# Optimization experiments

Measured on AMD Instinct MI355X. Metric: run time of the kernel, lower is better.

The kernel has to match this reference:

```python
import jax, jax.numpy as jnp
from jax import lax
import numpy as np

T, B, D, N = 1024, 32, 1024, 64
INIT_D_ALPHA, INIT_ALPHA_BIAS = 0.1, 2.0

def _xavier(key, n_out, n_in):
    lim = float(np.sqrt(6.0 / (n_in + n_out)))
    return jax.random.uniform(key, (n_out, n_in), jnp.float32, -lim, lim)

def setup_inputs() -> dict:
    key = jax.random.key(0)
    k = jax.random.split(key, 5)
    return {
        "x": jax.random.normal(k[0], (T, B, D), jnp.float32),
        "S0": jnp.zeros((B, N, N), jnp.float32),
        "W_k": _xavier(k[1], N, D),
        "W_v": _xavier(k[2], N, D),
        "W_q": _xavier(k[3], N, D),
        "W_alpha": _xavier(k[4], N, D),
        "d_alpha": jnp.full((N,), INIT_D_ALPHA, jnp.float32),
        "b_alpha": jnp.full((N,), INIT_ALPHA_BIAS, jnp.float32),
    }

def reference(x, S0, W_k, W_v, W_q, W_alpha, d_alpha, b_alpha):
    # Precompute all per-step projections as batched GEMMs: [T,B,N]
    k = jnp.einsum('tbd,nd->tbn', x, W_k)
    v = jnp.einsum('tbd,nd->tbn', x, W_v)
    q = jnp.einsum('tbd,nd->tbn', x, W_q)
    ax = jnp.einsum('tbd,nd->tbn', x, W_alpha)

    def step(S, inp):
        k_t, v_t, q_t, ax_t = inp  # each [B,N]
        retrieved = jnp.einsum('bij,bj->bi', S, k_t)            # S @ k
        alpha = jax.nn.sigmoid(ax_t + d_alpha * retrieved + b_alpha)  # [B,N]
        outer = v_t[:, :, None] * k_t[:, None, :]               # outer(v,k) [B,N,N]
        S = alpha[:, :, None] * S + (1.0 - alpha)[:, :, None] * outer
        h = jnp.einsum('bij,bj->bi', S, q_t)                    # S @ q
        out = h * jax.nn.silu(h)                                # self-gated
        return S, out

    S_final, output = lax.scan(step, S0, (k, v, q, ax))
    return output, S_final
```

## Files before the change

### kernel.cpp

```cpp
#include <hip/hip_runtime.h>
#include <math.h>

#define T_STEPS 1024
#define BATCH   32
#define DIM     1024
#define NST     64
#define TBN     ((size_t)T_STEPS * BATCH * NST)

typedef __attribute__((ext_vector_type(8))) short bf16x8;
typedef __attribute__((ext_vector_type(4))) float f32x4;


__device__ __forceinline__ void gload16(const float* g, float* l)
{
    __builtin_amdgcn_global_load_lds(
        (const __attribute__((address_space(1))) unsigned int*)g,
        (__attribute__((address_space(3))) unsigned int*)l, 16, 0, 0);
}

__device__ __forceinline__ void cvt8(float4 v0, float4 v1, bf16x8& hi, bf16x8& lo)
{
    float f[8] = {v0.x, v0.y, v0.z, v0.w, v1.x, v1.y, v1.z, v1.w};
    bf16x8 h, l;
    #pragma unroll
    for (int i = 0; i < 8; i++) {
        unsigned b = __float_as_uint(f[i]);
        h[i] = (short)(b >> 16);
        l[i] = (short)(__float_as_uint(f[i] - __uint_as_float(b & 0xffff0000u)) >> 16);
    }
    hi = h; lo = l;
}

__global__ __launch_bounds__(512, 1)
void proj_gemm_v2(const float* __restrict__ x,
                  const float* __restrict__ Wk,
                  const float* __restrict__ Wv,
                  const float* __restrict__ Wq,
                  const float* __restrict__ Wa,
                  const float* __restrict__ b_alpha,
                  float* __restrict__ ws)
{
    __shared__ float As[2][128][32];
    __shared__ float Bs[2][256][32];

    const int tid  = threadIdx.x;
    const int lane = tid & 63;
    const int w    = tid >> 6;
    const int m0   = blockIdx.x * 128;

    const int lrow  = lane >> 3;
    const int lgran = (lane & 7) ^ lrow;
    const float* ap0 = x + (size_t)(m0 + 16*w +     lrow) * DIM + lgran * 4;
    const float* ap1 = x + (size_t)(m0 + 16*w + 8 + lrow) * DIM + lgran * 4;
    const float* Wsrc = (w < 2) ? Wk : (w < 4) ? Wv : (w < 6) ? Wq : Wa;
    const float* bp0 = Wsrc + (size_t)((w & 1)*32 +  0 + lrow) * DIM + lgran * 4;
    const float* bp1 = Wsrc + (size_t)((w & 1)*32 +  8 + lrow) * DIM + lgran * 4;
    const float* bp2 = Wsrc + (size_t)((w & 1)*32 + 16 + lrow) * DIM + lgran * 4;
    const float* bp3 = Wsrc + (size_t)((w & 1)*32 + 24 + lrow) * DIM + lgran * 4;

    auto stage = [&](int kb, int buf) {
        const int ko = kb * 32;
        gload16(ap0 + ko, &As[buf][16*w     ][0]);
        gload16(ap1 + ko, &As[buf][16*w +  8][0]);
        gload16(bp0 + ko, &Bs[buf][32*w     ][0]);
        gload16(bp1 + ko, &Bs[buf][32*w +  8][0]);
        gload16(bp2 + ko, &Bs[buf][32*w + 16][0]);
        gload16(bp3 + ko, &Bs[buf][32*w + 24][0]);
    };

    const int fr = lane & 15;
    const int qi = lane >> 4;
    const int sx = fr & 7;
    const int mh = w >> 2;
    const int nq = w & 3;

    f32x4 acc[4][4];
    #pragma unroll
    for (int i = 0; i < 4; i++)
        #pragma unroll
        for (int j = 0; j < 4; j++)
            acc[i][j] = (f32x4)0.0f;

    stage(0, 0);
    __syncthreads();

    #pragma unroll 1
    for (int kb = 0; kb < 32; kb++) {
        const int buf = kb & 1;
        if (kb + 1 < 32) stage(kb + 1, buf ^ 1);

        bf16x8 ah[4], al[4], bh[4], bl[4];
        #pragma unroll
        for (int mt = 0; mt < 4; mt++) {
            const float* rp = &As[buf][mh*64 + mt*16 + fr][0];
            float4 v0 = *(const float4*)(rp + (((2*qi    ) ^ sx) * 4));
            float4 v1 = *(const float4*)(rp + (((2*qi + 1) ^ sx) * 4));
            cvt8(v0, v1, ah[mt], al[mt]);
        }
        #pragma unroll
        for (int nt = 0; nt < 4; nt++) {
            const float* rp = &Bs[buf][nq*64 + nt*16 + fr][0];
            float4 v0 = *(const float4*)(rp + (((2*qi    ) ^ sx) * 4));
            float4 v1 = *(const float4*)(rp + (((2*qi + 1) ^ sx) * 4));
            cvt8(v0, v1, bh[nt], bl[nt]);
        }
        #pragma unroll
        for (int mt = 0; mt < 4; mt++)
            #pragma unroll
            for (int nt = 0; nt < 4; nt++) {
                acc[mt][nt] = __builtin_amdgcn_mfma_f32_16x16x32_bf16(ah[mt], bh[nt], acc[mt][nt], 0, 0, 0);
                acc[mt][nt] = __builtin_amdgcn_mfma_f32_16x16x32_bf16(al[mt], bh[nt], acc[mt][nt], 0, 0, 0);
                acc[mt][nt] = __builtin_amdgcn_mfma_f32_16x16x32_bf16(ah[mt], bl[nt], acc[mt][nt], 0, 0, 0);
            }

        __syncthreads();
    }

    float* outb = ws + (size_t)nq * TBN;
    const int r0 = qi * 4;
    float bav[4];
    #pragma unroll
    for (int nt = 0; nt < 4; nt++)
        bav[nt] = (nq == 3) ? b_alpha[nt*16 + fr] : 0.0f;
    #pragma unroll
    for (int mt = 0; mt < 4; mt++)
        #pragma unroll
        for (int nt = 0; nt < 4; nt++)
            #pragma unroll
            for (int r = 0; r < 4; r++)
                outb[(size_t)(m0 + mh*64 + mt*16 + r0 + r) * NST + nt*16 + fr]
                    = acc[mt][nt][r] + bav[nt];
}


template <int CTRL>
__device__ __forceinline__ float dpp_add(float v) {
    int o = __builtin_amdgcn_mov_dpp(__float_as_int(v), CTRL, 0xF, 0xF, true);
    return v + __int_as_float(o);
}
__device__ __forceinline__ float reduce16(float v) {
    v = dpp_add<0xB1>(v);
    v = dpp_add<0x4E>(v);
    v = dpp_add<0x141>(v);
    v = dpp_add<0x140>(v);
    return v;
}
__device__ __forceinline__ float fast_sigmoid(float z) {
    float e = __builtin_amdgcn_exp2f(z * -1.44269504088896340736f);
    return __builtin_amdgcn_rcpf(1.0f + e);
}

#define SCH 16
#define NCH (T_STEPS / SCH)

__global__ __launch_bounds__(64, 1)
void scan16_kernel(const float* __restrict__ ws,
                   const float* __restrict__ S0,
                   const float* __restrict__ d_alpha,
                   float* __restrict__ out)
{
    const float* kb_ = ws;
    const float* vb_ = ws + TBN;
    const float* qb_ = ws + 2 * TBN;
    const float* ab_ = ws + 3 * TBN;

    __shared__ float kq[2][SCH][128];
    __shared__ float va[2][SCH][8];
    __shared__ float dd[SCH];

    const int lane = threadIdx.x;
    const int bid = blockIdx.x;
    const int b   = (bid & 7) * 4 + ((bid >> 3) & 3);
    const int rg  = bid >> 5;
    const int rl  = lane >> 4;
    const int cl  = lane & 15;
    const int row = rg * 4 + rl;
    const int c0  = cl * 4;

    float S[4];
    {
        float4 sv = *(const float4*)(S0 + ((size_t)b * NST + row) * NST + c0);
        S[0] = sv.x; S[1] = sv.y; S[2] = sv.z; S[3] = sv.w;
    }
    const float da = d_alpha[row];

    const size_t stp = (size_t)BATCH * NST;

    int kqs[8], kqf[8];
    const float* kqg[8];
    #pragma unroll
    for (int p = 0; p < 8; p++) {
        const int idx = p * 64 + lane;
        const int s   = idx >> 5;
        const int f   = idx & 31;
        kqs[p] = s; kqf[p] = f;
        kqg[p] = ((f < 16) ? kb_ : qb_) + (size_t)s * stp + (size_t)b * NST + (f & 15) * 4;
    }
    const int vas = (lane & 31) >> 1;
    const int vaw = lane & 1;
    const float* vag = (vaw ? ab_ : vb_) + (size_t)vas * stp + (size_t)b * NST + rg * 4;

    auto issue = [&](int ch, float4 (&rk)[8], float4& rv) {
        const size_t off = (size_t)ch * SCH * stp;
        #pragma unroll
        for (int p = 0; p < 8; p++)
            rk[p] = *(const float4*)(kqg[p] + off);
        rv = *(const float4*)(vag + off);
    };
    auto commit = [&](int bi, const float4 (&rk)[8], const float4& rv) {
        #pragma unroll
        for (int p = 0; p < 8; p++)
            *(float4*)&kq[bi][kqs[p]][kqf[p] * 4] = rk[p];
        if (lane < 32)
            *(float4*)&va[bi][vas][vaw * 4] = rv;
    };

    {
        float4 rk[8]; float4 rv;
        issue(0, rk, rv); commit(0, rk, rv);
        issue(1, rk, rv); commit(1, rk, rv);
    }

    float kc[4], kn[4];
    *(float4*)kc = *(const float4*)&kq[0][0][c0];
    *(float4*)kn = *(const float4*)&kq[0][1][c0];
    float qf_c[4];
    *(float4*)qf_c = *(const float4*)&kq[0][0][64 + c0];
    float vv_c = va[0][0][rl];
    float aa_c = va[0][0][4 + rl];

    float ret;
    {
        float p0 = fmaf(S[1], kc[1], S[0] * kc[0]) + fmaf(S[3], kc[3], S[2] * kc[2]);
        ret = reduce16(p0);
    }

    float* op = out + (size_t)b * NST + row;

    for (int ch = 0; ch < NCH; ch++) {
        const int cur = ch & 1, nxt = cur ^ 1;

        float4 rk[8]; float4 rv;
        const int cn = (ch + 2 < NCH) ? ch + 2 : NCH - 1;
        issue(cn, rk, rv);

        {
            const int tl = lane & 15;
            const int qg = lane >> 4;
            const float* kt = &kq[cur][tl][0];
            const float* knp = (tl < 15) ? &kq[cur][tl + 1][0] : &kq[nxt][0][0];
            float dsum = 0.0f;
            #pragma unroll
            for (int i = 0; i < 4; i++) {
                const int g = ((qg * 4 + i + tl) & 15) * 4;
                float4 a = *(const float4*)(kt + g);
                float4 c = *(const float4*)(knp + g);
                dsum = fmaf(a.x, c.x, dsum); dsum = fmaf(a.y, c.y, dsum);
                dsum = fmaf(a.z, c.z, dsum); dsum = fmaf(a.w, c.w, dsum);
            }
            dsum += __shfl_xor(dsum, 16);
            dsum += __shfl_xor(dsum, 32);
            if (lane < 16) dd[lane] = dsum;
        }

        #pragma unroll
        for (int s = 0; s < SCH; s++) {
            const int t = ch * SCH + s;

            float qf_n[4], kn2[4], vv_n, aa_n;
            if (s < SCH - 1) {
                *(float4*)qf_n = *(const float4*)&kq[cur][s + 1][64 + c0];
                vv_n = va[cur][s + 1][rl];
                aa_n = va[cur][s + 1][4 + rl];
            } else {
                *(float4*)qf_n = *(const float4*)&kq[nxt][0][64 + c0];
                vv_n = va[nxt][0][rl];
                aa_n = va[nxt][0][4 + rl];
            }
            if (s < SCH - 2)       *(float4*)kn2 = *(const float4*)&kq[cur][s + 2][c0];
            else if (s == SCH - 2) *(float4*)kn2 = *(const float4*)&kq[nxt][0][c0];
            else                   *(float4*)kn2 = *(const float4*)&kq[nxt][1][c0];

            const float d2v = dd[s];

            const float z     = fmaf(da, ret, aa_c);
            const float alpha = fast_sigmoid(z);

            float d1 = fmaf(S[1], kn[1], S[0] * kn[0]) + fmaf(S[3], kn[3], S[2] * kn[2]);
            d1 = reduce16(d1);

            const float w = (1.f - alpha) * vv_c;
            S[0] = fmaf(alpha, S[0], w * kc[0]);
            S[1] = fmaf(alpha, S[1], w * kc[1]);
            S[2] = fmaf(alpha, S[2], w * kc[2]);
            S[3] = fmaf(alpha, S[3], w * kc[3]);

            const float c2v = vv_c * d2v;
            ret = fmaf(alpha, d1 - c2v, c2v);

            float h = fmaf(S[1], qf_c[1], S[0] * qf_c[0]) + fmaf(S[3], qf_c[3], S[2] * qf_c[2]);
            h = reduce16(h);
            const float o = h * h * fast_sigmoid(h);
            if (cl == 0) op[(size_t)t * stp] = o;

            kc[0] = kn[0]; kc[1] = kn[1]; kc[2] = kn[2]; kc[3] = kn[3];
            kn[0] = kn2[0]; kn[1] = kn2[1]; kn[2] = kn2[2]; kn[3] = kn2[3];
            qf_c[0] = qf_n[0]; qf_c[1] = qf_n[1]; qf_c[2] = qf_n[2]; qf_c[3] = qf_n[3];
            vv_c = vv_n; aa_c = aa_n;
        }

        commit(cur, rk, rv);
    }

    float* sfp = out + TBN + ((size_t)b * NST + row) * NST + c0;
    *(float4*)sfp = make_float4(S[0], S[1], S[2], S[3]);
}


extern "C" void kernel_launch(void* const* d_in, const int* in_sizes, int n_in,
                              void* d_out, int out_size, void* d_ws, size_t ws_size,
                              hipStream_t stream)
{
    const float* x  = (const float*)d_in[0];
    const float* S0 = (const float*)d_in[1];
    const float* Wk = (const float*)d_in[2];
    const float* Wv = (const float*)d_in[3];
    const float* Wq = (const float*)d_in[4];
    const float* Wa = (const float*)d_in[5];
    const float* da = (const float*)d_in[6];
    const float* ba = (const float*)d_in[7];
    float* out = (float*)d_out;
    float* ws  = (float*)d_ws;

    proj_gemm_v2<<<dim3((T_STEPS * BATCH) / 128), 512, 0, stream>>>(x, Wk, Wv, Wq, Wa, ba, ws);

    scan16_kernel<<<dim3(BATCH * 16), 64, 0, stream>>>(ws, S0, da, out);
}
```

Baseline: 408.7 us.

## Deepen retrieval recurrence lookahead to two steps and batch output reductions

```diff
diff --git a/kernel.cpp b/kernel.cpp
--- a/kernel.cpp
+++ b/kernel.cpp
@@ -9,6 +9,8 @@
 
 typedef __attribute__((ext_vector_type(8))) short bf16x8;
 typedef __attribute__((ext_vector_type(4))) float f32x4;
+
+#define NLOG2E (-1.44269504088896340736f)
 
 
 __device__ __forceinline__ void gload16(const float* g, float* l)
@@ -122,6 +124,7 @@
     #pragma unroll
     for (int nt = 0; nt < 4; nt++)
         bav[nt] = (nq == 3) ? b_alpha[nt*16 + fr] : 0.0f;
+    const float scl = (nq == 3) ? NLOG2E : 1.0f;
     #pragma unroll
     for (int mt = 0; mt < 4; mt++)
         #pragma unroll
@@ -129,7 +132,7 @@
             #pragma unroll
             for (int r = 0; r < 4; r++)
                 outb[(size_t)(m0 + mh*64 + mt*16 + r0 + r) * NST + nt*16 + fr]
-                    = acc[mt][nt][r] + bav[nt];
+                    = (acc[mt][nt][r] + bav[nt]) * scl;
 }
 
 
@@ -145,9 +148,18 @@
     v = dpp_add<0x140>(v);
     return v;
 }
-__device__ __forceinline__ float fast_sigmoid(float z) {
-    float e = __builtin_amdgcn_exp2f(z * -1.44269504088896340736f);
+__device__ __forceinline__ void reduce16x4(float& a, float& b, float& c, float& d) {
+    a = dpp_add<0xB1>(a);  b = dpp_add<0xB1>(b);  c = dpp_add<0xB1>(c);  d = dpp_add<0xB1>(d);
+    a = dpp_add<0x4E>(a);  b = dpp_add<0x4E>(b);  c = dpp_add<0x4E>(c);  d = dpp_add<0x4E>(d);
+    a = dpp_add<0x141>(a); b = dpp_add<0x141>(b); c = dpp_add<0x141>(c); d = dpp_add<0x141>(d);
+    a = dpp_add<0x140>(a); b = dpp_add<0x140>(b); c = dpp_add<0x140>(c); d = dpp_add<0x140>(d);
+}
+__device__ __forceinline__ float fast_sigmoid(float h) {
+    float e = __builtin_amdgcn_exp2f(h * NLOG2E);
     return __builtin_amdgcn_rcpf(1.0f + e);
+}
+__device__ __forceinline__ float dot4(const float* a, const float* b) {
+    return fmaf(a[1], b[1], a[0] * b[0]) + fmaf(a[3], b[3], a[2] * b[2]);
 }
 
 #define SCH 16
@@ -166,7 +178,7 @@
 
     __shared__ float kq[2][SCH][128];
     __shared__ float va[2][SCH][8];
-    __shared__ float dd[SCH];
+    __shared__ float ddt[SCH], eet[SCH];
 
     const int lane = threadIdx.x;
     const int bid = blockIdx.x;
@@ -182,7 +194,7 @@
         float4 sv = *(const float4*)(S0 + ((size_t)b * NST + row) * NST + c0);
         S[0] = sv.x; S[1] = sv.y; S[2] = sv.z; S[3] = sv.w;
     }
-    const float da = d_alpha[row];
+    const float da_s = d_alpha[row] * NLOG2E;
 
     const size_t stp = (size_t)BATCH * NST;
 
@@ -221,22 +233,25 @@
         issue(1, rk, rv); commit(1, rk, rv);
     }
 
-    float kc[4], kn[4];
-    *(float4*)kc = *(const float4*)&kq[0][0][c0];
-    *(float4*)kn = *(const float4*)&kq[0][1][c0];
-    float qf_c[4];
+    float kc[4], kn[4], kn2[4];
+    *(float4*)kc  = *(const float4*)&kq[0][0][c0];
+    *(float4*)kn  = *(const float4*)&kq[0][1][c0];
+    *(float4*)kn2 = *(const float4*)&kq[0][2][c0];
+    float qf_c[4], qf_n[4];
     *(float4*)qf_c = *(const float4*)&kq[0][0][64 + c0];
-    float vv_c = va[0][0][rl];
-    float aa_c = va[0][0][4 + rl];
-
-    float ret;
-    {
-        float p0 = fmaf(S[1], kc[1], S[0] * kc[0]) + fmaf(S[3], kc[3], S[2] * kc[2]);
-        ret = reduce16(p0);
-    }
-
+    *(float4*)qf_n = *(const float4*)&kq[0][1][64 + c0];
+    float vv_c = va[0][0][rl], aa_c = va[0][0][4 + rl];
+    float vv_n = va[0][1][rl], aa_n = va[0][1][4 + rl];
+
+    float a1 = 1.0f, oma1 = 0.0f, vprev = 0.0f, eev_carry = 0.0f;
+    float gg = 0.0f;
+    float u  = reduce16(dot4(S, kc));
+    float RD = reduce16(dot4(S, kn));
+
+    float hp[4];
     float* op = out + (size_t)b * NST + row;
 
+    #pragma unroll 1
     for (int ch = 0; ch < NCH; ch++) {
         const int cur = ch & 1, nxt = cur ^ 1;
 
@@ -247,68 +262,99 @@
         {
             const int tl = lane & 15;
             const int qg = lane >> 4;
-            const float* kt = &kq[cur][tl][0];
-            const float* knp = (tl < 15) ? &kq[cur][tl + 1][0] : &kq[nxt][0][0];
-            float dsum = 0.0f;
+            const float* k0p = &kq[cur][tl][0];
+            const float* k1p = (tl < 15) ? &kq[cur][tl + 1][0] : &kq[nxt][0][0];
+            const float* k2p = (tl < 14) ? &kq[cur][tl + 2][0] : &kq[nxt][tl - 14][0];
+            float ds = 0.0f, es = 0.0f;
             #pragma unroll
             for (int i = 0; i < 4; i++) {
                 const int g = ((qg * 4 + i + tl) & 15) * 4;
-                float4 a = *(const float4*)(kt + g);
-                float4 c = *(const float4*)(knp + g);
-                dsum = fmaf(a.x, c.x, dsum); dsum = fmaf(a.y, c.y, dsum);
-                dsum = fmaf(a.z, c.z, dsum); dsum = fmaf(a.w, c.w, dsum);
+                float4 a  = *(const float4*)(k0p + g);
+                float4 b1 = *(const float4*)(k1p + g);
+                float4 c  = *(const float4*)(k2p + g);
+                ds = fmaf(a.x, b1.x, ds); ds = fmaf(a.y, b1.y, ds);
+                ds = fmaf(a.z, b1.z, ds); ds = fmaf(a.w, b1.w, ds);
+                es = fmaf(a.x, c.x, es);  es = fmaf(a.y, c.y, es);
+                es = fmaf(a.z, c.z, es);  es = fmaf(a.w, c.w, es);
             }
-            dsum += __shfl_xor(dsum, 16);
-            dsum += __shfl_xor(dsum, 32);
-            if (lane < 16) dd[lane] = dsum;
+            ds += __shfl_xor(ds, 16); ds += __shfl_xor(ds, 32);
+            es += __shfl_xor(es, 16); es += __shfl_xor(es, 32);
+            if (lane < 16) { ddt[lane] = ds; eet[lane] = es; }
+        }
+        float ddRa[16], eeRa[16];
+        #pragma unroll
+        for (int j = 0; j < 4; j++) {
+            *(float4*)&ddRa[4*j] = *(const float4*)&ddt[4*j];
+            *(float4*)&eeRa[4*j] = *(const float4*)&eet[4*j];
         }
 
         #pragma unroll
         for (int s = 0; s < SCH; s++) {
             const int t = ch * SCH + s;
 
-            float qf_n[4], kn2[4], vv_n, aa_n;
-            if (s < SCH - 1) {
-                *(float4*)qf_n = *(const float4*)&kq[cur][s + 1][64 + c0];
-                vv_n = va[cur][s + 1][rl];
-                aa_n = va[cur][s + 1][4 + rl];
+            const float ret = fmaf(a1, gg, u);
+            const float z   = fmaf(da_s, ret, aa_c);
+            const float e   = __builtin_amdgcn_exp2f(z);
+
+            float k3[4], qn2[4], vv2, aa2;
+            if (s + 3 < SCH) *(float4*)k3 = *(const float4*)&kq[cur][s + 3][c0];
+            else             *(float4*)k3 = *(const float4*)&kq[nxt][s + 3 - SCH][c0];
+            if (s + 2 < SCH) {
+                *(float4*)qn2 = *(const float4*)&kq[cur][s + 2][64 + c0];
+                vv2 = va[cur][s + 2][rl]; aa2 = va[cur][s + 2][4 + rl];
             } else {
-                *(float4*)qf_n = *(const float4*)&kq[nxt][0][64 + c0];
-                vv_n = va[nxt][0][rl];
-                aa_n = va[nxt][0][4 + rl];
+                *(float4*)qn2 = *(const float4*)&kq[nxt][s + 2 - SCH][64 + c0];
+                vv2 = va[nxt][s + 2 - SCH][rl]; aa2 = va[nxt][s + 2 - SCH][4 + rl];
             }
-            if (s < SCH - 2)       *(float4*)kn2 = *(const float4*)&kq[cur][s + 2][c0];
-            else if (s == SCH - 2) *(float4*)kn2 = *(const float4*)&kq[nxt][0][c0];
-            else                   *(float4*)kn2 = *(const float4*)&kq[nxt][1][c0];
-
-            const float d2v = dd[s];
-
-            const float z     = fmaf(da, ret, aa_c);
-            const float alpha = fast_sigmoid(z);
-
-            float d1 = fmaf(S[1], kn[1], S[0] * kn[0]) + fmaf(S[3], kn[3], S[2] * kn[2]);
-            d1 = reduce16(d1);
-
-            const float w = (1.f - alpha) * vv_c;
+
+            const float ddv = ddRa[s];
+            const float eev = (s == 0) ? eev_carry : eeRa[s - 1];
+            const float w1  = oma1 * vprev * eev;
+            const float P   = fmaf(a1, RD, w1);
+            const float u_n = vv_c * ddv;
+            const float gg_n = P - u_n;
+
+            float qp = dot4(S, kn2);
+            const float RD_n = reduce16(qp);
+
+            const float alpha = __builtin_amdgcn_rcpf(1.0f + e);
+
+            const float oma = 1.0f - alpha;
+            const float w   = oma * vv_c;
             S[0] = fmaf(alpha, S[0], w * kc[0]);
             S[1] = fmaf(alpha, S[1], w * kc[1]);
             S[2] = fmaf(alpha, S[2], w * kc[2]);
             S[3] = fmaf(alpha, S[3], w * kc[3]);
 
-            const float c2v = vv_c * d2v;
-            ret = fmaf(alpha, d1 - c2v, c2v);
-
-            float h = fmaf(S[1], qf_c[1], S[0] * qf_c[0]) + fmaf(S[3], qf_c[3], S[2] * qf_c[2]);
-            h = reduce16(h);
-            const float o = h * h * fast_sigmoid(h);
-            if (cl == 0) op[(size_t)t * stp] = o;
-
-            kc[0] = kn[0]; kc[1] = kn[1]; kc[2] = kn[2]; kc[3] = kn[3];
+            hp[s & 3] = dot4(S, qf_c);
+            if ((s & 3) == 3) {
+                float h0 = hp[0], h1 = hp[1], h2 = hp[2], h3 = hp[3];
+                reduce16x4(h0, h1, h2, h3);
+                const float o0 = h0 * h0 * fast_sigmoid(h0);
+                const float o1 = h1 * h1 * fast_sigmoid(h1);
+                const float o2 = h2 * h2 * fast_sigmoid(h2);
+                const float o3 = h3 * h3 * fast_sigmoid(h3);
+                if (cl == 0) {
+                    op[(size_t)(t - 3) * stp] = o0;
+                    op[(size_t)(t - 2) * stp] = o1;
+                    op[(size_t)(t - 1) * stp] = o2;
+                    op[(size_t)(t    ) * stp] = o3;
+                }
+            }
+
+            a1 = alpha; oma1 = oma; vprev = vv_c;
+            u = u_n; gg = gg_n;
+            float RDt = RD_n; (void)RDt;
+            kc[0] = kn[0];  kc[1] = kn[1];  kc[2] = kn[2];  kc[3] = kn[3];
             kn[0] = kn2[0]; kn[1] = kn2[1]; kn[2] = kn2[2]; kn[3] = kn2[3];
+            kn2[0] = k3[0]; kn2[1] = k3[1]; kn2[2] = k3[2]; kn2[3] = k3[3];
             qf_c[0] = qf_n[0]; qf_c[1] = qf_n[1]; qf_c[2] = qf_n[2]; qf_c[3] = qf_n[3];
-            vv_c = vv_n; aa_c = aa_n;
-        }
-
+            qf_n[0] = qn2[0];  qf_n[1] = qn2[1];  qf_n[2] = qn2[2];  qf_n[3] = qn2[3];
+            vv_c = vv_n; aa_c = aa_n; vv_n = vv2; aa_n = aa2;
+            RD = RD_n;
+        }
+
+        eev_carry = eeRa[15];
         commit(cur, rk, rv);
     }
 
```

Measured after the change: 416.6 us. No clear change (+1.9%).

## Chunked Gram-matrix scan with MFMA retrieval and output projections

Applied to the files above, without the earlier changes.

```diff
diff --git a/kernel.cpp b/kernel.cpp
--- a/kernel.cpp
+++ b/kernel.cpp
@@ -9,6 +9,13 @@
 
 typedef __attribute__((ext_vector_type(8))) short bf16x8;
 typedef __attribute__((ext_vector_type(4))) float f32x4;
+
+#define NLOG2E (-1.44269504088896340736f)
+
+__device__ unsigned short g_khi[TBN];
+__device__ unsigned short g_klo[TBN];
+__device__ unsigned short g_qhi[TBN];
+__device__ unsigned short g_qlo[TBN];
 
 
 __device__ __forceinline__ void gload16(const float* g, float* l)
@@ -122,198 +129,179 @@
     #pragma unroll
     for (int nt = 0; nt < 4; nt++)
         bav[nt] = (nq == 3) ? b_alpha[nt*16 + fr] : 0.0f;
+    const float scl = (nq == 3) ? NLOG2E : 1.0f;
     #pragma unroll
     for (int mt = 0; mt < 4; mt++)
         #pragma unroll
         for (int nt = 0; nt < 4; nt++)
             #pragma unroll
-            for (int r = 0; r < 4; r++)
-                outb[(size_t)(m0 + mh*64 + mt*16 + r0 + r) * NST + nt*16 + fr]
-                    = acc[mt][nt][r] + bav[nt];
-}
-
-
-template <int CTRL>
-__device__ __forceinline__ float dpp_add(float v) {
-    int o = __builtin_amdgcn_mov_dpp(__float_as_int(v), CTRL, 0xF, 0xF, true);
-    return v + __int_as_float(o);
-}
-__device__ __forceinline__ float reduce16(float v) {
-    v = dpp_add<0xB1>(v);
-    v = dpp_add<0x4E>(v);
-    v = dpp_add<0x141>(v);
-    v = dpp_add<0x140>(v);
-    return v;
-}
-__device__ __forceinline__ float fast_sigmoid(float z) {
-    float e = __builtin_amdgcn_exp2f(z * -1.44269504088896340736f);
-    return __builtin_amdgcn_rcpf(1.0f + e);
-}
+            for (int r = 0; r < 4; r++) {
+                const float val = (acc[mt][nt][r] + bav[nt]) * scl;
+                const size_t idx = (size_t)(m0 + mh*64 + mt*16 + r0 + r) * NST + nt*16 + fr;
+                if (nq != 2)
+                    outb[idx] = val;
+                if (nq == 0 || nq == 2) {
+                    const unsigned bits = __float_as_uint(val);
+                    const unsigned short hi = (unsigned short)(bits >> 16);
+                    const float lof = val - __uint_as_float(bits & 0xffff0000u);
+                    const unsigned short lo = (unsigned short)(__float_as_uint(lof) >> 16);
+                    if (nq == 0) { g_khi[idx] = hi; g_klo[idx] = lo; }
+                    else         { g_qhi[idx] = hi; g_qlo[idx] = lo; }
+                }
+            }
+}
+
 
 #define SCH 16
 #define NCH (T_STEPS / SCH)
 
-__global__ __launch_bounds__(64, 1)
-void scan16_kernel(const float* __restrict__ ws,
-                   const float* __restrict__ S0,
-                   const float* __restrict__ d_alpha,
-                   float* __restrict__ out)
+__global__ __launch_bounds__(256, 2)
+void scan_gram(const float* __restrict__ ws,
+               const float* __restrict__ S0,
+               const float* __restrict__ d_alpha,
+               float* __restrict__ out)
 {
     const float* kb_ = ws;
     const float* vb_ = ws + TBN;
-    const float* qb_ = ws + 2 * TBN;
     const float* ab_ = ws + 3 * TBN;
 
-    __shared__ float kq[2][SCH][128];
-    __shared__ float va[2][SCH][8];
-    __shared__ float dd[SCH];
-
-    const int lane = threadIdx.x;
-    const int bid = blockIdx.x;
-    const int b   = (bid & 7) * 4 + ((bid >> 3) & 3);
-    const int rg  = bid >> 5;
-    const int rl  = lane >> 4;
-    const int cl  = lane & 15;
-    const int row = rg * 4 + rl;
-    const int c0  = cl * 4;
-
-    float S[4];
-    {
-        float4 sv = *(const float4*)(S0 + ((size_t)b * NST + row) * NST + c0);
-        S[0] = sv.x; S[1] = sv.y; S[2] = sv.z; S[3] = sv.w;
+    __shared__ float k_st[2][SCH][64];
+    __shared__ float va  [2][SCH][16];
+    __shared__ float G_lds [SCH][16];
+    __shared__ float GQ_lds[SCH][16];
+    __shared__ float S_pvt[4][64];
+
+    const int tid  = threadIdx.x;
+    const int lane = tid & 63;
+    const int w    = tid >> 6;
+    const int bid  = blockIdx.x;
+    const int b    = (bid & 7) * 4 + ((bid >> 3) & 3);
+    const int rg   = bid >> 5;
+    const int row  = rg * 4 + w;
+    const int fr   = lane & 15;
+    const int qi   = lane >> 4;
+
+    const size_t stp = (size_t)BATCH * NST;
+
+    float S = S0[((size_t)b * NST + row) * NST + lane];
+    const float da_s = d_alpha[row] * NLOG2E;
+
+    const float* ksrc = kb_ + (size_t)(4*w + qi) * stp + (size_t)b * NST + fr * 4;
+    const float* vsrc = ((lane & 1) ? ab_ : vb_)
+                      + (size_t)(lane >> 2) * stp + (size_t)b * NST + rg * 4;
+
+    auto stage = [&](int ch, int buf) {
+        gload16(ksrc + (size_t)ch * SCH * stp, &k_st[buf][4*w][0]);
+        if (w == 0)
+            gload16(vsrc + (size_t)ch * SCH * stp, &va[buf][0][0]);
+    };
+
+    stage(0, 0);
+    __syncthreads();
+
+    float* op = out + (size_t)b * NST + row;
+    float R = 0.0f, H = 0.0f, hv = 0.0f;
+
+    #pragma unroll 1
+    for (int ch = 0; ch < NCH; ch++) {
+        const int buf = ch & 1;
+        if (ch + 1 < NCH) stage(ch + 1, buf ^ 1);
+
+        const size_t fb = (size_t)ch * SCH * stp + (size_t)fr * stp + (size_t)b * NST + qi * 8;
+        const bf16x8 Kh0 = *(const bf16x8*)(g_khi + fb);
+        const bf16x8 Kh1 = *(const bf16x8*)(g_khi + fb + 32);
+        const bf16x8 Kl0 = *(const bf16x8*)(g_klo + fb);
+        const bf16x8 Kl1 = *(const bf16x8*)(g_klo + fb + 32);
+        const bf16x8 Qh0 = *(const bf16x8*)(g_qhi + fb);
+        const bf16x8 Qh1 = *(const bf16x8*)(g_qhi + fb + 32);
+        const bf16x8 Ql0 = *(const bf16x8*)(g_qlo + fb);
+        const bf16x8 Ql1 = *(const bf16x8*)(g_qlo + fb + 32);
+
+        S_pvt[w][lane] = S;
+        bf16x8 Sh0, Sl0, Sh1, Sl1;
+        {
+            float4 s0 = *(const float4*)&S_pvt[w][qi * 8];
+            float4 s1 = *(const float4*)&S_pvt[w][qi * 8 + 4];
+            cvt8(s0, s1, Sh0, Sl0);
+            float4 s2 = *(const float4*)&S_pvt[w][32 + qi * 8];
+            float4 s3 = *(const float4*)&S_pvt[w][32 + qi * 8 + 4];
+            cvt8(s2, s3, Sh1, Sl1);
+        }
+
+        f32x4 aG = (f32x4)0.0f, aGQ = (f32x4)0.0f;
+        f32x4 aR0 = (f32x4)0.0f, aR1 = (f32x4)0.0f;
+        f32x4 aH0 = (f32x4)0.0f, aH1 = (f32x4)0.0f;
+
+        aG = __builtin_amdgcn_mfma_f32_16x16x32_bf16(Kh0, Kh0, aG, 0, 0, 0);
+        aG = __builtin_amdgcn_mfma_f32_16x16x32_bf16(Kh0, Kl0, aG, 0, 0, 0);
+        aG = __builtin_amdgcn_mfma_f32_16x16x32_bf16(Kl0, Kh0, aG, 0, 0, 0);
+        aG = __builtin_amdgcn_mfma_f32_16x16x32_bf16(Kh1, Kh1, aG, 0, 0, 0);
+        aG = __builtin_amdgcn_mfma_f32_16x16x32_bf16(Kh1, Kl1, aG, 0, 0, 0);
+        aG = __builtin_amdgcn_mfma_f32_16x16x32_bf16(Kl1, Kh1, aG, 0, 0, 0);
+
+        aGQ = __builtin_amdgcn_mfma_f32_16x16x32_bf16(Kh0, Qh0, aGQ, 0, 0, 0);
+        aGQ = __builtin_amdgcn_mfma_f32_16x16x32_bf16(Kh0, Ql0, aGQ, 0, 0, 0);
+        aGQ = __builtin_amdgcn_mfma_f32_16x16x32_bf16(Kl0, Qh0, aGQ, 0, 0, 0);
+        aGQ = __builtin_amdgcn_mfma_f32_16x16x32_bf16(Kh1, Qh1, aGQ, 0, 0, 0);
+        aGQ = __builtin_amdgcn_mfma_f32_16x16x32_bf16(Kh1, Ql1, aGQ, 0, 0, 0);
+        aGQ = __builtin_amdgcn_mfma_f32_16x16x32_bf16(Kl1, Qh1, aGQ, 0, 0, 0);
+
+        aR0 = __builtin_amdgcn_mfma_f32_16x16x32_bf16(Sh0, Kh0, aR0, 0, 0, 0);
+        aR0 = __builtin_amdgcn_mfma_f32_16x16x32_bf16(Sh0, Kl0, aR0, 0, 0, 0);
+        aR0 = __builtin_amdgcn_mfma_f32_16x16x32_bf16(Sl0, Kh0, aR0, 0, 0, 0);
+        aR1 = __builtin_amdgcn_mfma_f32_16x16x32_bf16(Sh1, Kh1, aR1, 0, 0, 0);
+        aR1 = __builtin_amdgcn_mfma_f32_16x16x32_bf16(Sh1, Kl1, aR1, 0, 0, 0);
+        aR1 = __builtin_amdgcn_mfma_f32_16x16x32_bf16(Sl1, Kh1, aR1, 0, 0, 0);
+
+        aH0 = __builtin_amdgcn_mfma_f32_16x16x32_bf16(Sh0, Qh0, aH0, 0, 0, 0);
+        aH0 = __builtin_amdgcn_mfma_f32_16x16x32_bf16(Sh0, Ql0, aH0, 0, 0, 0);
+        aH0 = __builtin_amdgcn_mfma_f32_16x16x32_bf16(Sl0, Qh0, aH0, 0, 0, 0);
+        aH1 = __builtin_amdgcn_mfma_f32_16x16x32_bf16(Sh1, Qh1, aH1, 0, 0, 0);
+        aH1 = __builtin_amdgcn_mfma_f32_16x16x32_bf16(Sh1, Ql1, aH1, 0, 0, 0);
+        aH1 = __builtin_amdgcn_mfma_f32_16x16x32_bf16(Sl1, Qh1, aH1, 0, 0, 0);
+
+        #pragma unroll
+        for (int r = 0; r < 4; r++) {
+            G_lds [qi*4 + r][fr] = aG[r];
+            GQ_lds[qi*4 + r][fr] = aGQ[r];
+        }
+        R = aR0[0] + aR1[0];
+        H = aH0[0] + aH1[0];
+
+        #pragma unroll
+        for (int s = 0; s < SCH; s++) {
+            const float kcv = k_st[buf][s][lane];
+            const float Gv  = G_lds [s][fr];
+            const float GQv = GQ_lds[s][fr];
+            const float vv  = va[buf][s][w];
+            const float aa  = va[buf][s][4 + w];
+
+            const float ret   = __int_as_float(
+                __builtin_amdgcn_readlane(__float_as_int(R), s));
+            const float z     = fmaf(da_s, ret, aa);
+            const float e     = __builtin_amdgcn_exp2f(z);
+            const float alpha = __builtin_amdgcn_rcpf(1.0f + e);
+            const float bt    = (1.0f - alpha) * vv;
+
+            R = fmaf(alpha, R, bt * Gv);
+            H = fmaf(alpha, H, bt * GQv);
+            S = fmaf(alpha, S, bt * kcv);
+
+            hv = (lane == s) ? H : hv;
+        }
+
+        {
+            const float zz = hv * NLOG2E;
+            const float sg = __builtin_amdgcn_rcpf(1.0f + __builtin_amdgcn_exp2f(zz));
+            const float o  = hv * hv * sg;
+            if (lane < SCH)
+                op[(size_t)(ch * SCH + lane) * stp] = o;
+        }
+
+        __syncthreads();
     }
-    const float da = d_alpha[row];
-
-    const size_t stp = (size_t)BATCH * NST;
-
-    int kqs[8], kqf[8];
-    const float* kqg[8];
-    #pragma unroll
-    for (int p = 0; p < 8; p++) {
-        const int idx = p * 64 + lane;
-        const int s   = idx >> 5;
-        const int f   = idx & 31;
-        kqs[p] = s; kqf[p] = f;
-        kqg[p] = ((f < 16) ? kb_ : qb_) + (size_t)s * stp + (size_t)b * NST + (f & 15) * 4;
-    }
-    const int vas = (lane & 31) >> 1;
-    const int vaw = lane & 1;
-    const float* vag = (vaw ? ab_ : vb_) + (size_t)vas * stp + (size_t)b * NST + rg * 4;
-
-    auto issue = [&](int ch, float4 (&rk)[8], float4& rv) {
-        const size_t off = (size_t)ch * SCH * stp;
-        #pragma unroll
-        for (int p = 0; p < 8; p++)
-            rk[p] = *(const float4*)(kqg[p] + off);
-        rv = *(const float4*)(vag + off);
-    };
-    auto commit = [&](int bi, const float4 (&rk)[8], const float4& rv) {
-        #pragma unroll
-        for (int p = 0; p < 8; p++)
-            *(float4*)&kq[bi][kqs[p]][kqf[p] * 4] = rk[p];
-        if (lane < 32)
-            *(float4*)&va[bi][vas][vaw * 4] = rv;
-    };
-
-    {
-        float4 rk[8]; float4 rv;
-        issue(0, rk, rv); commit(0, rk, rv);
-        issue(1, rk, rv); commit(1, rk, rv);
-    }
-
-    float kc[4], kn[4];
-    *(float4*)kc = *(const float4*)&kq[0][0][c0];
-    *(float4*)kn = *(const float4*)&kq[0][1][c0];
-    float qf_c[4];
-    *(float4*)qf_c = *(const float4*)&kq[0][0][64 + c0];
-    float vv_c = va[0][0][rl];
-    float aa_c = va[0][0][4 + rl];
-
-    float ret;
-    {
-        float p0 = fmaf(S[1], kc[1], S[0] * kc[0]) + fmaf(S[3], kc[3], S[2] * kc[2]);
-        ret = reduce16(p0);
-    }
-
-    float* op = out + (size_t)b * NST + row;
-
-    for (int ch = 0; ch < NCH; ch++) {
-        const int cur = ch & 1, nxt = cur ^ 1;
-
-        float4 rk[8]; float4 rv;
-        const int cn = (ch + 2 < NCH) ? ch + 2 : NCH - 1;
-        issue(cn, rk, rv);
-
-        {
-            const int tl = lane & 15;
-            const int qg = lane >> 4;
-            const float* kt = &kq[cur][tl][0];
-            const float* knp = (tl < 15) ? &kq[cur][tl + 1][0] : &kq[nxt][0][0];
-            float dsum = 0.0f;
-            #pragma unroll
-            for (int i = 0; i < 4; i++) {
-                const int g = ((qg * 4 + i + tl) & 15) * 4;
-                float4 a = *(const float4*)(kt + g);
-                float4 c = *(const float4*)(knp + g);
-                dsum = fmaf(a.x, c.x, dsum); dsum = fmaf(a.y, c.y, dsum);
-                dsum = fmaf(a.z, c.z, dsum); dsum = fmaf(a.w, c.w, dsum);
-            }
-            dsum += __shfl_xor(dsum, 16);
-            dsum += __shfl_xor(dsum, 32);
-            if (lane < 16) dd[lane] = dsum;
-        }
-
-        #pragma unroll
-        for (int s = 0; s < SCH; s++) {
-            const int t = ch * SCH + s;
-
-            float qf_n[4], kn2[4], vv_n, aa_n;
-            if (s < SCH - 1) {
-                *(float4*)qf_n = *(const float4*)&kq[cur][s + 1][64 + c0];
-                vv_n = va[cur][s + 1][rl];
-                aa_n = va[cur][s + 1][4 + rl];
-            } else {
-                *(float4*)qf_n = *(const float4*)&kq[nxt][0][64 + c0];
-                vv_n = va[nxt][0][rl];
-                aa_n = va[nxt][0][4 + rl];
-            }
-            if (s < SCH - 2)       *(float4*)kn2 = *(const float4*)&kq[cur][s + 2][c0];
-            else if (s == SCH - 2) *(float4*)kn2 = *(const float4*)&kq[nxt][0][c0];
-            else                   *(float4*)kn2 = *(const float4*)&kq[nxt][1][c0];
-
-            const float d2v = dd[s];
-
-            const float z     = fmaf(da, ret, aa_c);
-            const float alpha = fast_sigmoid(z);
-
-            float d1 = fmaf(S[1], kn[1], S[0] * kn[0]) + fmaf(S[3], kn[3], S[2] * kn[2]);
-            d1 = reduce16(d1);
-
-            const float w = (1.f - alpha) * vv_c;
-            S[0] = fmaf(alpha, S[0], w * kc[0]);
-            S[1] = fmaf(alpha, S[1], w * kc[1]);
-            S[2] = fmaf(alpha, S[2], w * kc[2]);
-            S[3] = fmaf(alpha, S[3], w * kc[3]);
-
-            const float c2v = vv_c * d2v;
-            ret = fmaf(alpha, d1 - c2v, c2v);
-
-            float h = fmaf(S[1], qf_c[1], S[0] * qf_c[0]) + fmaf(S[3], qf_c[3], S[2] * qf_c[2]);
-            h = reduce16(h);
-            const float o = h * h * fast_sigmoid(h);
-            if (cl == 0) op[(size_t)t * stp] = o;
-
-            kc[0] = kn[0]; kc[1] = kn[1]; kc[2] = kn[2]; kc[3] = kn[3];
-            kn[0] = kn2[0]; kn[1] = kn2[1]; kn[2] = kn2[2]; kn[3] = kn2[3];
-            qf_c[0] = qf_n[0]; qf_c[1] = qf_n[1]; qf_c[2] = qf_n[2]; qf_c[3] = qf_n[3];
-            vv_c = vv_n; aa_c = aa_n;
-        }
-
-        commit(cur, rk, rv);
-    }
-
-    float* sfp = out + TBN + ((size_t)b * NST + row) * NST + c0;
-    *(float4*)sfp = make_float4(S[0], S[1], S[2], S[3]);
+
+    out[TBN + ((size_t)b * NST + row) * NST + lane] = S;
 }
 
 
@@ -334,5 +322,5 @@
 
     proj_gemm_v2<<<dim3((T_STEPS * BATCH) / 128), 512, 0, stream>>>(x, Wk, Wv, Wq, Wa, ba, ws);
 
-    scan16_kernel<<<dim3(BATCH * 16), 64, 0, stream>>>(ws, S0, da, out);
-}
+    scan_gram<<<dim3(BATCH * 16), 256, 0, stream>>>(ws, S0, da, out);
+}
```

Result: slower. 436.1 us (+6.7%).
